# Kernel optimization log

Measured on AMD Instinct MI355X. Metric: run time of the kernel, lower is better.

Reference implementation:

```python
import jax, jax.numpy as jnp
import numpy as np

NI = 256        # in_channels
QK = NI // 8    # query/key channels = 32
BS, H, W = 4, 64, 64


def setup_inputs() -> dict:
    key = jax.random.key(0)
    ks = jax.random.split(key, 8)
    x = jax.random.normal(ks[0], (BS, NI, H, W), dtype=jnp.float32)
    # 1x1 conv weights stored as [out_ch, in_ch] (kernel is 1x1)
    wq = jax.random.normal(ks[1], (QK, NI), dtype=jnp.float32) * (1.0 / np.sqrt(NI))
    bq = jnp.zeros((QK,), dtype=jnp.float32)
    wk = jax.random.normal(ks[2], (QK, NI), dtype=jnp.float32) * (1.0 / np.sqrt(NI))
    bk = jnp.zeros((QK,), dtype=jnp.float32)
    wv = jax.random.normal(ks[3], (NI, NI), dtype=jnp.float32) * (1.0 / np.sqrt(NI))
    bv = jnp.zeros((NI,), dtype=jnp.float32)
    # gamma is zero-init in the module; use small random values so the
    # attention branch actually contributes (post-training state).
    gamma = jax.random.normal(ks[4], (1, NI, 1, 1), dtype=jnp.float32) * 0.1
    return {"x": x, "wq": wq, "bq": bq, "wk": wk, "bk": bk,
            "wv": wv, "bv": bv, "gamma": gamma}


def reference(x, wq, bq, wk, bk, wv, bv, gamma):
    bs, c, h, w = x.shape
    n = h * w
    xf = x.reshape(bs, c, n)                       # [bs, c, N]
    # 1x1 convs == per-pixel linear maps over channels
    q = jnp.einsum('oc,bcn->bno', wq, xf) + bq     # [bs, N, qk]
    k = jnp.einsum('oc,bcn->bon', wk, xf) + bk[None, :, None]  # [bs, qk, N]
    v = jnp.einsum('oc,bcn->bon', wv, xf) + bv[None, :, None]  # [bs, c, N]
    attn = jax.nn.softmax(jnp.einsum('bnq,bqm->bnm', q, k), axis=-1)  # [bs, N, N]
    out = jnp.einsum('bcm,bnm->bcn', v, attn)      # value @ attn^T
    out = out.reshape(bs, c, h, w)
    return gamma * out + x
```

## Files before the change

kernel.cpp:

```cpp
#include <hip/hip_runtime.h>
#include <cstdint>
#include <cstddef>

#define NI   256
#define QKC  32
#define BS   4
#define NPIX 4096
#define LOG2E 1.4426950408889634f

typedef __bf16 bf16x8 __attribute__((ext_vector_type(8)));
typedef __bf16 bf16x4 __attribute__((ext_vector_type(4)));
typedef float  f32x16 __attribute__((ext_vector_type(16)));

__device__ inline f32x16 zero16() {
    f32x16 z;
    #pragma unroll
    for (int i = 0; i < 16; ++i) z[i] = 0.f;
    return z;
}

__global__ __launch_bounds__(256) void wconv_pack(
    const float* __restrict__ wq, const float* __restrict__ wk,
    const float* __restrict__ wv, __bf16* __restrict__ wpk)
{
    int f = blockIdx.x * 256 + threadIdx.x;
    int otl = f >> 10, rem = f & 1023;
    int kk = rem >> 6, h = (rem >> 5) & 1, l31 = rem & 31;
    int och = otl * 32 + l31, c0 = kk * 16 + 8 * h;
    const float* src = och < 32 ? wq + och * NI + c0
                     : och < 64 ? wk + (och - 32) * NI + c0
                                : wv + (och - 64) * NI + c0;
    float4 x0 = *(const float4*)src;
    float4 x1 = *(const float4*)(src + 4);
    __align__(16) __bf16 o8[8] = {
        (__bf16)x0.x, (__bf16)x0.y, (__bf16)x0.z, (__bf16)x0.w,
        (__bf16)x1.x, (__bf16)x1.y, (__bf16)x1.z, (__bf16)x1.w};
    *(uint4*)(wpk + (size_t)f * 8) = *(const uint4*)o8;
}

__global__ __launch_bounds__(256) void qkv_mfma(
    const float* __restrict__ x, const __bf16* __restrict__ wpk,
    const float* __restrict__ bq, const float* __restrict__ bk,
    const float* __restrict__ bv,
    __bf16* __restrict__ qpk, __bf16* __restrict__ kpk, __bf16* __restrict__ vpk)
{
    __shared__ __align__(16) __bf16 xT[32][264];
    __shared__ float bls[320];

    const int t = threadIdx.x, w = t >> 6, lane = t & 63;
    const int l31 = lane & 31, h = lane >> 5;
    const int b = blockIdx.y, n0 = blockIdx.x * 32, kt = blockIdx.x;

    for (int i = t; i < 320; i += 256)
        bls[i] = i < 32 ? bq[i] : i < 64 ? bk[i - 32] : bv[i - 64];

    {
        int n4 = (t & 7) * 4, cb = (t >> 3) * 8;
        float4 xv[8];
        #pragma unroll
        for (int j = 0; j < 8; ++j)
            xv[j] = *(const float4*)(x + ((size_t)(b * NI) + cb + j) * NPIX + n0 + n4);
        #pragma unroll
        for (int i = 0; i < 4; ++i) {
            __align__(16) __bf16 r8[8];
            #pragma unroll
            for (int j = 0; j < 8; ++j) r8[j] = (__bf16)((&xv[j].x)[i]);
            *(uint4*)&xT[n4 + i][cb] = *(const uint4*)r8;
        }
    }
    __syncthreads();

    f32x16 acc[3] = {zero16(), zero16(), zero16()};
    #pragma unroll 4
    for (int kk = 0; kk < 16; ++kk) {
        bf16x8 xf = *(const bf16x8*)&xT[l31][kk * 16 + 8 * h];
        #pragma unroll
        for (int jj = 0; jj < 3; ++jj) {
            int otl = w + 4 * jj;
            if (otl < 10) {
                bf16x8 wf = *(const bf16x8*)(wpk + (size_t)((otl * 16 + kk) * 64 + 32 * h + l31) * 8);
                acc[jj] = __builtin_amdgcn_mfma_f32_32x32x16_bf16(wf, xf, acc[jj], 0, 0, 0);
            }
        }
    }
    __syncthreads();

    __bf16 (*vT)[264] = xT;
    #pragma unroll
    for (int jj = 0; jj < 3; ++jj) {
        int otl = w + 4 * jj;
        if (otl >= 2 && otl < 10) {
            #pragma unroll
            for (int qd = 0; qd < 4; ++qd) {
                int c0v = (otl - 2) * 32 + 8 * qd + 4 * h;
                __align__(8) __bf16 q4[4];
                #pragma unroll
                for (int i = 0; i < 4; ++i)
                    q4[i] = (__bf16)(acc[jj][4 * qd + i] + bls[64 + c0v + i]);
                *(uint2*)&vT[l31][c0v] = *(const uint2*)q4;
            }
        }
    }
    #pragma unroll
    for (int jj = 0; jj < 3; ++jj) {
        int otl = w + 4 * jj;
        if (otl == 0) {
            #pragma unroll
            for (int kc = 0; kc < 2; ++kc) {
                __align__(16) __bf16 hi8[8], lo8[8];
                #pragma unroll
                for (int j = 0; j < 8; ++j) {
                    int r = 8 * kc + j;
                    int och = (r & 3) + 8 * (r >> 2) + 4 * h;
                    float val = (acc[jj][r] + bls[och]) * LOG2E;
                    __bf16 hh = (__bf16)val;
                    hi8[j] = hh;
                    lo8[j] = (__bf16)(val - (float)hh);
                }
                size_t base = ((((size_t)(b * 128 + kt) * 2 + 0) * 2 + kc) * 2 + h) * 32 + l31;
                *(uint4*)(qpk + base * 8) = *(const uint4*)hi8;
                size_t basel = ((((size_t)(b * 128 + kt) * 2 + 1) * 2 + kc) * 2 + h) * 32 + l31;
                *(uint4*)(qpk + basel * 8) = *(const uint4*)lo8;
            }
        } else if (otl == 1) {
            #pragma unroll
            for (int kc = 0; kc < 2; ++kc) {
                __align__(16) __bf16 k8[8];
                #pragma unroll
                for (int j = 0; j < 8; ++j) {
                    int r = 8 * kc + j;
                    int och = (r & 3) + 8 * (r >> 2) + 4 * h;
                    k8[j] = (__bf16)(acc[jj][r] + bls[32 + och]);
                }
                size_t base = (((size_t)(b * 128 + kt) * 2 + h) * 32 + l31) * 2 + kc;
                *(uint4*)(kpk + base * 8) = *(const uint4*)k8;
            }
        }
    }
    __syncthreads();

    #pragma unroll
    for (int kc = 0; kc < 2; ++kc)
        #pragma unroll
        for (int hh = 0; hh < 2; ++hh) {
            __align__(16) __bf16 f8[8];
            #pragma unroll
            for (int j = 0; j < 8; ++j) f8[j] = vT[16 * kc + 8 * hh + j][t];
            size_t base = (((((size_t)(b * 64 + (kt >> 1)) * 2 + hh) * 256 + t) * 2
                            + (kt & 1)) * 2 + kc);
            *(uint4*)(vpk + base * 8) = *(const uint4*)f8;
        }
}

template <int NSP>
__global__ __launch_bounds__(512, 4) void attn_mfma(
    const __bf16* __restrict__ qpk, const __bf16* __restrict__ kpk,
    const __bf16* __restrict__ vpk,
    __bf16* __restrict__ Opart, float* __restrict__ dpart)
{
    constexpr int MTT = 64 / NSP;
    constexpr int J   = MTT / 2;
    __shared__ __align__(16) __bf16 pt_f[4][2][4][64][8];
    __shared__ float dwave[8][32];

    const int t = threadIdx.x;
    const int b = blockIdx.x & 3, ksp = blockIdx.x >> 2;
    const int n0 = blockIdx.y * 64;
    const int w = t >> 6, lane = t & 63, l31 = lane & 31, h = lane >> 5;
    const int q = w & 3, sr = q & 1, sc = q >> 1, pp = w >> 2;
    const int kt0 = ksp * (128 / NSP);

    const int qt = 2 * blockIdx.y + sr;
    bf16x8 qf[2][2];
    #pragma unroll
    for (int hl = 0; hl < 2; ++hl)
        #pragma unroll
        for (int kc = 0; kc < 2; ++kc)
            qf[hl][kc] = *(const bf16x8*)(qpk +
                (((((size_t)(b * 128 + qt) * 2 + hl) * 2 + kc) * 2 + h) * 32 + l31) * 8);

    const size_t kinv = (size_t)b * 131072 + (size_t)h * 512 + (size_t)l31 * 16;
    const size_t vinv = (size_t)b * 1048576 + (size_t)h * 8192
                      + (size_t)(32 * w + l31) * 32;

    auto kload = [&](int ktile, int kc) {
        return *(const bf16x8*)(kpk + kinv + (size_t)ktile * 1024 + kc * 8);
    };

    f32x16 a0 = zero16(), a1 = zero16();
    float dacc = 0.f;

    auto smma = [&](bf16x8 kh0, bf16x8 kh1) {
        f32x16 s = zero16();
        __builtin_amdgcn_s_setprio(1);
        s = __builtin_amdgcn_mfma_f32_32x32x16_bf16(kh0, qf[0][0], s, 0, 0, 0);
        s = __builtin_amdgcn_mfma_f32_32x32x16_bf16(kh1, qf[0][1], s, 0, 0, 0);
        s = __builtin_amdgcn_mfma_f32_32x32x16_bf16(kh0, qf[1][0], s, 0, 0, 0);
        s = __builtin_amdgcn_mfma_f32_32x32x16_bf16(kh1, qf[1][1], s, 0, 0, 0);
        __builtin_amdgcn_s_setprio(0);
        return s;
    };

    auto sfin = [&](const f32x16& s, int buf) {
        unsigned xw[8], xs[8];
        #pragma unroll
        for (int i = 0; i < 8; ++i) {
            float e0 = __builtin_amdgcn_exp2f(s[2 * i]);
            float e1 = __builtin_amdgcn_exp2f(s[2 * i + 1]);
            dacc += e0 + e1;
            __align__(4) __bf16 pr[2] = {(__bf16)e0, (__bf16)e1};
            xw[i] = *(const unsigned*)pr;
        }
        #pragma unroll
        for (int i = 0; i < 8; ++i) xs[i] = __shfl_xor(xw[i], 32);
        const bool hi = (h != 0);
        __align__(16) unsigned f0[4], f1[4];
        f0[0] = hi ? xs[2] : xw[0];  f0[1] = hi ? xs[3] : xw[1];
        f0[2] = hi ? xw[2] : xs[0];  f0[3] = hi ? xw[3] : xs[1];
        f1[0] = hi ? xs[6] : xw[4];  f1[1] = hi ? xs[7] : xw[5];
        f1[2] = hi ? xw[6] : xs[4];  f1[3] = hi ? xw[7] : xs[5];
        *(uint4*)&pt_f[buf][sr][2 * sc + 0][lane][0] = *(const uint4*)f0;
        *(uint4*)&pt_f[buf][sr][2 * sc + 1][lane][0] = *(const uint4*)f1;
    };

    auto pvblock = [&](int mt, const bf16x8 (*vf)[2]) {
        const int buf = mt & 3;
        __builtin_amdgcn_s_setprio(1);
        #pragma unroll
        for (int i = 0; i < 2; ++i)
            #pragma unroll
            for (int kc = 0; kc < 2; ++kc) {
                const int s2 = 2 * i + kc;
                bf16x8 pa0 = *(const bf16x8*)&pt_f[buf][0][s2][lane][0];
                bf16x8 pa1 = *(const bf16x8*)&pt_f[buf][1][s2][lane][0];
                a0 = __builtin_amdgcn_mfma_f32_32x32x16_bf16(pa0, vf[i][kc], a0, 0, 0, 0);
                a1 = __builtin_amdgcn_mfma_f32_32x32x16_bf16(pa1, vf[i][kc], a1, 0, 0, 0);
            }
        __builtin_amdgcn_s_setprio(0);
    };

    bf16x8 kh0 = kload(kt0 + 2 * pp + sc, 0), kh1 = kload(kt0 + 2 * pp + sc, 1);
    {
        f32x16 s = smma(kh0, kh1);
        sfin(s, pp);
    }
    kh0 = kload(kt0 + 2 * (2 + pp) + sc, 0);
    kh1 = kload(kt0 + 2 * (2 + pp) + sc, 1);
    __syncthreads();

    for (int j = 0; j < J; ++j) {
        f32x16 s;
        if (j < J - 1) s = smma(kh0, kh1);

        const __bf16* va = vpk + vinv + (size_t)(ksp * MTT + 2 * j) * 16384;
        bf16x8 vfa[2][2];
        #pragma unroll
        for (int i = 0; i < 2; ++i)
            #pragma unroll
            for (int kc = 0; kc < 2; ++kc)
                vfa[i][kc] = *(const bf16x8*)(va + i * 16 + kc * 8);

        if (j < J - 2) {
            const int mtsn = 2 * j + 4 + pp;
            kh0 = kload(kt0 + 2 * mtsn + sc, 0);
            kh1 = kload(kt0 + 2 * mtsn + sc, 1);
        }
        if (j < J - 1) sfin(s, (2 * j + 2 + pp) & 3);

        bf16x8 vfb[2][2];
        #pragma unroll
        for (int i = 0; i < 2; ++i)
            #pragma unroll
            for (int kc = 0; kc < 2; ++kc)
                vfb[i][kc] = *(const bf16x8*)(va + 16384 + i * 16 + kc * 8);

        pvblock(2 * j, vfa);
        pvblock(2 * j + 1, vfb);
        __syncthreads();
    }

    float dtot = dacc + __shfl_xor(dacc, 32);
    if (lane < 32) dwave[w][l31] = dtot;
    __syncthreads();
    if (w < 2 && lane < 32) {
        float dsum = dwave[w][l31] + dwave[w + 2][l31]
                   + dwave[w + 4][l31] + dwave[w + 6][l31];
        dpart[((size_t)(ksp * BS + b)) * NPIX + n0 + 32 * w + l31] = dsum;
    }

    size_t obase = (((size_t)(ksp * BS + b)) * NI + 32 * w + l31) * NPIX + n0;
    #pragma unroll
    for (int rq = 0; rq < 4; ++rq) {
        int nn = 8 * rq + 4 * h;
        __align__(8) __bf16 t0[4], t1[4];
        #pragma unroll
        for (int i = 0; i < 4; ++i) {
            t0[i] = (__bf16)a0[4 * rq + i];
            t1[i] = (__bf16)a1[4 * rq + i];
        }
        *(uint2*)(Opart + obase + nn)      = *(const uint2*)t0;
        *(uint2*)(Opart + obase + 32 + nn) = *(const uint2*)t1;
    }
}

template <int NSP>
__global__ __launch_bounds__(256) void combine(
    const float* __restrict__ x, const float* __restrict__ gamma,
    const __bf16* __restrict__ Opart, const float* __restrict__ dpart,
    float* __restrict__ out)
{
    int idx = (blockIdx.x * 256 + threadIdx.x) * 4;
    int n = idx & (NPIX - 1);
    int c = (idx >> 12) & (NI - 1);
    int b = idx >> 20;

    float4 osum = {0.f, 0.f, 0.f, 0.f};
    float4 dsum = {0.f, 0.f, 0.f, 0.f};
    #pragma unroll
    for (int p = 0; p < NSP; ++p) {
        bf16x4 pp = *(const bf16x4*)(Opart + (((size_t)(p * BS + b)) * NI + c) * NPIX + n);
        float4 dd = *(const float4*)(dpart + ((size_t)(p * BS + b)) * NPIX + n);
        osum.x += (float)pp[0]; osum.y += (float)pp[1];
        osum.z += (float)pp[2]; osum.w += (float)pp[3];
        dsum.x += dd.x; dsum.y += dd.y; dsum.z += dd.z; dsum.w += dd.w;
    }

    size_t xb = ((size_t)(b * NI) + c) * NPIX + n;
    float4 xv = *(const float4*)(x + xb);
    float g = gamma[c];

    float4 r;
    r.x = g * (osum.x / dsum.x) + xv.x;
    r.y = g * (osum.y / dsum.y) + xv.y;
    r.z = g * (osum.z / dsum.z) + xv.z;
    r.w = g * (osum.w / dsum.w) + xv.w;
    *(float4*)(out + xb) = r;
}

extern "C" void kernel_launch(void* const* d_in, const int* in_sizes, int n_in,
                              void* d_out, int out_size, void* d_ws, size_t ws_size,
                              hipStream_t stream)
{
    const float* x     = (const float*)d_in[0];
    const float* wq    = (const float*)d_in[1];
    const float* bq    = (const float*)d_in[2];
    const float* wk    = (const float*)d_in[3];
    const float* bk    = (const float*)d_in[4];
    const float* wv    = (const float*)d_in[5];
    const float* bv    = (const float*)d_in[6];
    const float* gamma = (const float*)d_in[7];
    float* out = (float*)d_out;

    const size_t WPK = (size_t)10240 * 8;
    const size_t QPK = (size_t)BS * 128 * 2 * 2 * 2 * 32 * 8;
    const size_t KPK = (size_t)BS * 128 * 2 * 2 * 32 * 8;
    const size_t VPK = (size_t)BS * 128 * 2 * 2 * 256 * 8;
    __bf16* wpk   = (__bf16*)d_ws;
    __bf16* qpk   = wpk + WPK;
    __bf16* kpk   = qpk + QPK;
    __bf16* vpk   = kpk + KPK;
    __bf16* Opart = vpk + VPK;

    wconv_pack<<<dim3(40), 256, 0, stream>>>(wq, wk, wv, wpk);
    qkv_mfma<<<dim3(NPIX / 32, BS), 256, 0, stream>>>(x, wpk, bq, bk, bv, qpk, kpk, vpk);

    const size_t OSZ4  = (size_t)4 * BS * NI * NPIX;
    const size_t need4 = (WPK + QPK + KPK + VPK + OSZ4) * sizeof(__bf16)
                       + (size_t)4 * BS * NPIX * sizeof(float);
    if (ws_size >= need4) {
        float* dpart = (float*)(Opart + OSZ4);
        attn_mfma<4><<<dim3(16, 64), 512, 0, stream>>>(qpk, kpk, vpk, Opart, dpart);
        combine<4><<<dim3(BS * NI * NPIX / 1024), 256, 0, stream>>>(x, gamma, Opart, dpart, out);
    } else {
        const size_t OSZ2 = (size_t)2 * BS * NI * NPIX;
        float* dpart = (float*)(Opart + OSZ2);
        attn_mfma<2><<<dim3(8, 64), 512, 0, stream>>>(qpk, kpk, vpk, Opart, dpart);
        combine<2><<<dim3(BS * NI * NPIX / 1024), 256, 0, stream>>>(x, gamma, Opart, dpart, out);
    }
}
```

Baseline: 165.4 us.

## Keep softmax probabilities in registers and split attention by channel half per wave

The attention kernel is restructured so each wave owns a 32-query chunk and a 128-channel half. The exponentiated probabilities now feed the PV MFMAs straight from registers, which removes the LDS staging buffer and the per-iteration block barriers. The V packing layout changes to match the new per-wave access pattern. The cost is that QK^T and exp are computed twice (once per channel half), and the software prefetch pipeline of K/V loads is dropped in favour of a simple loop.

```diff
diff --git a/kernel.cpp b/kernel.cpp
--- a/kernel.cpp
+++ b/kernel.cpp
@@ -146,51 +146,45 @@
             __align__(16) __bf16 f8[8];
             #pragma unroll
             for (int j = 0; j < 8; ++j) f8[j] = vT[16 * kc + 8 * hh + j][t];
-            size_t base = (((((size_t)(b * 64 + (kt >> 1)) * 2 + hh) * 256 + t) * 2
-                            + (kt & 1)) * 2 + kc);
+            size_t base = (((size_t)(b * 128 + kt) * 2 + hh) * 2 + kc) * 256 + t;
             *(uint4*)(vpk + base * 8) = *(const uint4*)f8;
         }
 }
 
-template <int NSP>
-__global__ __launch_bounds__(512, 4) void attn_mfma(
+template <int KSP>
+__global__ __launch_bounds__(256, 3) void attn_mfma(
     const __bf16* __restrict__ qpk, const __bf16* __restrict__ kpk,
     const __bf16* __restrict__ vpk,
     __bf16* __restrict__ Opart, float* __restrict__ dpart)
 {
-    constexpr int MTT = 64 / NSP;
-    constexpr int J   = MTT / 2;
-    __shared__ __align__(16) __bf16 pt_f[4][2][4][64][8];
-    __shared__ float dwave[8][32];
-
+    constexpr int NKT = 128 / KSP;
     const int t = threadIdx.x;
-    const int b = blockIdx.x & 3, ksp = blockIdx.x >> 2;
-    const int n0 = blockIdx.y * 64;
     const int w = t >> 6, lane = t & 63, l31 = lane & 31, h = lane >> 5;
-    const int q = w & 3, sr = q & 1, sc = q >> 1, pp = w >> 2;
-    const int kt0 = ksp * (128 / NSP);
-
-    const int qt = 2 * blockIdx.y + sr;
+    const int b = blockIdx.x & 3, ch = blockIdx.x >> 2;
+    const int nchunk = blockIdx.y * 4 + w;
+    const int ksp = blockIdx.z;
+    const int kt0 = ksp * NKT;
+
     bf16x8 qf[2][2];
     #pragma unroll
     for (int hl = 0; hl < 2; ++hl)
         #pragma unroll
         for (int kc = 0; kc < 2; ++kc)
             qf[hl][kc] = *(const bf16x8*)(qpk +
-                (((((size_t)(b * 128 + qt) * 2 + hl) * 2 + kc) * 2 + h) * 32 + l31) * 8);
-
-    const size_t kinv = (size_t)b * 131072 + (size_t)h * 512 + (size_t)l31 * 16;
-    const size_t vinv = (size_t)b * 1048576 + (size_t)h * 8192
-                      + (size_t)(32 * w + l31) * 32;
-
-    auto kload = [&](int ktile, int kc) {
-        return *(const bf16x8*)(kpk + kinv + (size_t)ktile * 1024 + kc * 8);
-    };
-
-    f32x16 a0 = zero16(), a1 = zero16();
+                (((((size_t)(b * 128 + nchunk) * 2 + hl) * 2 + kc) * 2 + h) * 32 + l31) * 8);
+
+    const __bf16* kp = kpk + (size_t)b * 131072 + (size_t)kt0 * 1024
+                     + (size_t)h * 512 + (size_t)l31 * 16;
+    const __bf16* vp = vpk + ((((size_t)(b * 128 + kt0) * 2 + h) * 2) * 256
+                     + 128 * ch + l31) * 8;
+
+    f32x16 D0 = zero16(), D1 = zero16(), D2 = zero16(), D3 = zero16();
     float dacc = 0.f;
 
-    auto smma = [&](bf16x8 kh0, bf16x8 kh1) {
+    for (int kt = 0; kt < NKT; ++kt) {
+        bf16x8 kh0 = *(const bf16x8*)(kp);
+        bf16x8 kh1 = *(const bf16x8*)(kp + 8);
+
         f32x16 s = zero16();
         __builtin_amdgcn_s_setprio(1);
         s = __builtin_amdgcn_mfma_f32_32x32x16_bf16(kh0, qf[0][0], s, 0, 0, 0);
@@ -198,10 +192,7 @@
         s = __builtin_amdgcn_mfma_f32_32x32x16_bf16(kh0, qf[1][0], s, 0, 0, 0);
         s = __builtin_amdgcn_mfma_f32_32x32x16_bf16(kh1, qf[1][1], s, 0, 0, 0);
         __builtin_amdgcn_s_setprio(0);
-        return s;
-    };
-
-    auto sfin = [&](const f32x16& s, int buf) {
+
         unsigned xw[8], xs[8];
         #pragma unroll
         for (int i = 0; i < 8; ++i) {
@@ -219,87 +210,42 @@
         f0[2] = hi ? xw[2] : xs[0];  f0[3] = hi ? xw[3] : xs[1];
         f1[0] = hi ? xs[6] : xw[4];  f1[1] = hi ? xs[7] : xw[5];
         f1[2] = hi ? xw[6] : xs[4];  f1[3] = hi ? xw[7] : xs[5];
-        *(uint4*)&pt_f[buf][sr][2 * sc + 0][lane][0] = *(const uint4*)f0;
-        *(uint4*)&pt_f[buf][sr][2 * sc + 1][lane][0] = *(const uint4*)f1;
-    };
-
-    auto pvblock = [&](int mt, const bf16x8 (*vf)[2]) {
-        const int buf = mt & 3;
+        bf16x8 pa0 = *(const bf16x8*)f0;
+        bf16x8 pa1 = *(const bf16x8*)f1;
+
         __builtin_amdgcn_s_setprio(1);
         #pragma unroll
-        for (int i = 0; i < 2; ++i)
-            #pragma unroll
-            for (int kc = 0; kc < 2; ++kc) {
-                const int s2 = 2 * i + kc;
-                bf16x8 pa0 = *(const bf16x8*)&pt_f[buf][0][s2][lane][0];
-                bf16x8 pa1 = *(const bf16x8*)&pt_f[buf][1][s2][lane][0];
-                a0 = __builtin_amdgcn_mfma_f32_32x32x16_bf16(pa0, vf[i][kc], a0, 0, 0, 0);
-                a1 = __builtin_amdgcn_mfma_f32_32x32x16_bf16(pa1, vf[i][kc], a1, 0, 0, 0);
-            }
+        for (int kcs = 0; kcs < 2; ++kcs) {
+            const bf16x8 pa = kcs ? pa1 : pa0;
+            const __bf16* vk = vp + kcs * 2048;
+            D0 = __builtin_amdgcn_mfma_f32_32x32x16_bf16(pa, *(const bf16x8*)(vk), D0, 0, 0, 0);
+            D1 = __builtin_amdgcn_mfma_f32_32x32x16_bf16(pa, *(const bf16x8*)(vk + 256), D1, 0, 0, 0);
+            D2 = __builtin_amdgcn_mfma_f32_32x32x16_bf16(pa, *(const bf16x8*)(vk + 512), D2, 0, 0, 0);
+            D3 = __builtin_amdgcn_mfma_f32_32x32x16_bf16(pa, *(const bf16x8*)(vk + 768), D3, 0, 0, 0);
+        }
         __builtin_amdgcn_s_setprio(0);
-    };
-
-    bf16x8 kh0 = kload(kt0 + 2 * pp + sc, 0), kh1 = kload(kt0 + 2 * pp + sc, 1);
-    {
-        f32x16 s = smma(kh0, kh1);
-        sfin(s, pp);
-    }
-    kh0 = kload(kt0 + 2 * (2 + pp) + sc, 0);
-    kh1 = kload(kt0 + 2 * (2 + pp) + sc, 1);
-    __syncthreads();
-
-    for (int j = 0; j < J; ++j) {
-        f32x16 s;
-        if (j < J - 1) s = smma(kh0, kh1);
-
-        const __bf16* va = vpk + vinv + (size_t)(ksp * MTT + 2 * j) * 16384;
-        bf16x8 vfa[2][2];
-        #pragma unroll
-        for (int i = 0; i < 2; ++i)
-            #pragma unroll
-            for (int kc = 0; kc < 2; ++kc)
-                vfa[i][kc] = *(const bf16x8*)(va + i * 16 + kc * 8);
-
-        if (j < J - 2) {
-            const int mtsn = 2 * j + 4 + pp;
-            kh0 = kload(kt0 + 2 * mtsn + sc, 0);
-            kh1 = kload(kt0 + 2 * mtsn + sc, 1);
-        }
-        if (j < J - 1) sfin(s, (2 * j + 2 + pp) & 3);
-
-        bf16x8 vfb[2][2];
-        #pragma unroll
-        for (int i = 0; i < 2; ++i)
-            #pragma unroll
-            for (int kc = 0; kc < 2; ++kc)
-                vfb[i][kc] = *(const bf16x8*)(va + 16384 + i * 16 + kc * 8);
-
-        pvblock(2 * j, vfa);
-        pvblock(2 * j + 1, vfb);
-        __syncthreads();
+
+        kp += 1024;
+        vp += 8192;
     }
 
     float dtot = dacc + __shfl_xor(dacc, 32);
-    if (lane < 32) dwave[w][l31] = dtot;
-    __syncthreads();
-    if (w < 2 && lane < 32) {
-        float dsum = dwave[w][l31] + dwave[w + 2][l31]
-                   + dwave[w + 4][l31] + dwave[w + 6][l31];
-        dpart[((size_t)(ksp * BS + b)) * NPIX + n0 + 32 * w + l31] = dsum;
-    }
-
-    size_t obase = (((size_t)(ksp * BS + b)) * NI + 32 * w + l31) * NPIX + n0;
-    #pragma unroll
-    for (int rq = 0; rq < 4; ++rq) {
-        int nn = 8 * rq + 4 * h;
-        __align__(8) __bf16 t0[4], t1[4];
-        #pragma unroll
-        for (int i = 0; i < 4; ++i) {
-            t0[i] = (__bf16)a0[4 * rq + i];
-            t1[i] = (__bf16)a1[4 * rq + i];
-        }
-        *(uint2*)(Opart + obase + nn)      = *(const uint2*)t0;
-        *(uint2*)(Opart + obase + 32 + nn) = *(const uint2*)t1;
+    if (ch == 0 && lane < 32)
+        dpart[((size_t)(ksp * BS + b)) * NPIX + nchunk * 32 + l31] = dtot;
+
+    const f32x16* Ds[4] = {&D0, &D1, &D2, &D3};
+    #pragma unroll
+    for (int cc = 0; cc < 4; ++cc) {
+        size_t obase = (((size_t)(ksp * BS + b)) * NI + 128 * ch + 32 * cc + l31) * NPIX
+                     + 32 * nchunk;
+        const f32x16& D = *Ds[cc];
+        #pragma unroll
+        for (int rq = 0; rq < 4; ++rq) {
+            __align__(8) __bf16 t4[4];
+            #pragma unroll
+            for (int i = 0; i < 4; ++i) t4[i] = (__bf16)D[4 * rq + i];
+            *(uint2*)(Opart + obase + 8 * rq + 4 * h) = *(const uint2*)t4;
+        }
     }
 }
 
@@ -369,12 +315,12 @@
                        + (size_t)4 * BS * NPIX * sizeof(float);
     if (ws_size >= need4) {
         float* dpart = (float*)(Opart + OSZ4);
-        attn_mfma<4><<<dim3(16, 64), 512, 0, stream>>>(qpk, kpk, vpk, Opart, dpart);
+        attn_mfma<4><<<dim3(8, 32, 4), 256, 0, stream>>>(qpk, kpk, vpk, Opart, dpart);
         combine<4><<<dim3(BS * NI * NPIX / 1024), 256, 0, stream>>>(x, gamma, Opart, dpart, out);
     } else {
         const size_t OSZ2 = (size_t)2 * BS * NI * NPIX;
         float* dpart = (float*)(Opart + OSZ2);
-        attn_mfma<2><<<dim3(8, 64), 512, 0, stream>>>(qpk, kpk, vpk, Opart, dpart);
+        attn_mfma<2><<<dim3(8, 32, 2), 256, 0, stream>>>(qpk, kpk, vpk, Opart, dpart);
         combine<2><<<dim3(BS * NI * NPIX / 1024), 256, 0, stream>>>(x, gamma, Opart, dpart, out);
     }
 }
```

New measurement: 213.4 us. +29.0%, slower.
